# Kernel tuning notes

Hardware: AMD Instinct MI355X
Metric: run time of the kernel (lower is better)

## Reference

```python
import jax, jax.numpy as jnp
import numpy as np

# Hyperparameters from __init__ defaults / chosen init kwargs
GAMMA_NEG = 4.0
GAMMA_POS = 1.0
CLIP = 0.05
EPS = 1e-8
ALPHA1 = 2.0
ALPHA_OTHER = 0.5
TOP_K = 10

B, C = 2048, 9605


def setup_inputs() -> dict:
    key = jax.random.key(0)
    k_x, k_y, k_c, k_r, k_d, k_o = jax.random.split(key, 6)
    x = jax.random.normal(k_x, (B, C), dtype=jnp.float32)
    y = (jax.random.uniform(k_y, (B, C)) < 0.01).astype(jnp.float32)
    compost_idx = jax.random.randint(k_c, (30,), 0, C, dtype=jnp.int32)
    recycle_idx = jax.random.randint(k_r, (70,), 0, C, dtype=jnp.int32)
    donate_idx = jax.random.randint(k_d, (70,), 0, C, dtype=jnp.int32)
    other_idx = jax.random.randint(k_o, (40,), 0, C, dtype=jnp.int32)
    # dense whitelist mapping: 0 = not in W_human mapping; priority compost>recycle>donate
    wl_map = jnp.zeros((C,), dtype=jnp.int32)
    wl_map = wl_map.at[other_idx].set(4)
    wl_map = wl_map.at[donate_idx].set(3)
    wl_map = wl_map.at[recycle_idx].set(2)
    wl_map = wl_map.at[compost_idx].set(1)
    return {"x": x, "y": y, "compost_idx": compost_idx,
            "recycle_idx": recycle_idx, "donate_idx": donate_idx,
            "wl_map": wl_map}


def reference(x, y, compost_idx, recycle_idx, donate_idx, wl_map):
    b, c = x.shape
    xs_pos = jax.nn.sigmoid(x)
    xs_neg = jnp.minimum(1.0 - xs_pos + CLIP, 1.0)  # clip shift, clamp max=1
    # base asymmetric BCE term: y*log(p) + (1-y)*log(1-p+clip)
    base = (y * jnp.log(jnp.maximum(xs_pos, EPS))
            + (1.0 - y) * jnp.log(jnp.maximum(xs_neg, EPS)))  # [B, C]

    # per-sample ground-truth whitelist groups (find_gt_whitelist)
    has1 = jnp.sum(y[:, compost_idx], axis=1) > 0  # [B]
    has2 = jnp.sum(y[:, recycle_idx], axis=1) > 0
    has3 = jnp.sum(y[:, donate_idx], axis=1) > 0
    gt_only4 = ~(has1 | has2 | has3)  # gt_whitelist == [4]

    # top-10 predicted classes (argsort descending, first 10)
    _, top_idx = jax.lax.top_k(xs_pos, TOP_K)  # [B, 10]
    rows = jnp.arange(b)

    def step(carry, j):
        # j: [B] class index at current rank; sequential over rank (order matters)
        mult, found = carry
        wl = wl_map[j]                      # group id of this class, 0 if unmapped
        in_map = wl > 0
        in_gt = (((wl == 1) & has1) | ((wl == 2) & has2)
                 | ((wl == 3) & has3) | ((wl == 4) & gt_only4))
        f = jnp.where(in_map & gt_only4, ALPHA_OTHER, 1.0)
        f = f * jnp.where(in_map & (~in_gt) & (~found), ALPHA1, 1.0)
        mult = mult.at[rows, j].multiply(f)
        found = found | (in_map & in_gt)
        return (mult, found), None

    init = (jnp.ones((b, c), x.dtype), jnp.zeros((b,), dtype=bool))
    (mult, found), _ = jax.lax.scan(step, init, top_idx.T)  # scan over 10 ranks

    # if no gt-whitelist match found in top-10: multiply all top-10 by alpha1 again
    extra = jnp.where(found[:, None], 1.0, ALPHA1)  # [B, 1]
    mult = mult.at[rows[:, None], top_idx].multiply(
        jnp.broadcast_to(extra, (b, TOP_K)))

    # asymmetric focal weighting (computed without grad in original)
    pt = xs_pos * y + xs_neg * (1.0 - y)
    gamma = GAMMA_POS * y + GAMMA_NEG * (1.0 - y)
    w = jax.lax.stop_gradient(jnp.power(1.0 - pt, gamma))

    return -jnp.sum(base * mult * w)
```

## Files before the change

### kernel.cpp

```cpp
#include <hip/hip_runtime.h>

#define TOPK 10
#define CLIP 0.05f
#define EPSV 1e-8f
#define ALPHA1 2.0f
#define ALPHA_OTHER 0.5f
#define TCAND 2.5f
#define MAXC 512

__device__ __forceinline__ unsigned long long pack_vc(float v, int c, int C) {
  unsigned u = __float_as_uint(v);
  unsigned key = (u & 0x80000000u) ? ~u : (u | 0x80000000u);
  return ((unsigned long long)key << 32) | (unsigned)(C - c);
}
__device__ __forceinline__ float unpack_v(unsigned long long p) {
  unsigned key = (unsigned)(p >> 32);
  unsigned u = (key & 0x80000000u) ? (key & 0x7fffffffu) : ~key;
  return __uint_as_float(u);
}
__device__ __forceinline__ int unpack_c(unsigned long long p, int C) {
  return C - (int)(unsigned)(p & 0xffffffffu);
}

__device__ __forceinline__ float base_w(float xv, bool pos) {
  float p = 1.f / (1.f + __expf(-xv));
  float xneg = fminf(1.f - p + CLIP, 1.f);
  float q = pos ? p : xneg;
  float b = __logf(fmaxf(q, EPSV));
  float t = 1.f - q;
  float t2 = t * t;
  float w = pos ? t : t2 * t2;
  return b * w;
}

__global__ __launch_bounds__(256) void asl_kernel(
    const float* __restrict__ x, const float* __restrict__ y,
    const int* __restrict__ compost, const int* __restrict__ recycle,
    const int* __restrict__ donate, const int* __restrict__ wl_map,
    float* __restrict__ out, int C, int n1, int n2, int n3)
{
  const int row = blockIdx.x;
  const float* xr = x + (size_t)row * (size_t)C;
  const float* yr = y + (size_t)row * (size_t)C;
  const int tid = threadIdx.x;
  const int lane = tid & 63;
  const int wave = tid >> 6;

  __shared__ int s_has[3];
  __shared__ unsigned s_cnt;
  __shared__ unsigned long long s_cand[MAXC];
  __shared__ float s_sum[4];
  __shared__ unsigned long long s_top[TOPK];

  if (tid < 3) s_has[tid] = 0;
  if (tid == 0) s_cnt = 0;
  __syncthreads();

  const int ntot = n1 + n2 + n3;
  for (int i = tid; i < ntot; i += 256) {
    int which, colI;
    if (i < n1)            { which = 0; colI = compost[i]; }
    else if (i < n1 + n2)  { which = 1; colI = recycle[i - n1]; }
    else                   { which = 2; colI = donate[i - n1 - n2]; }
    if (yr[colI] > 0.5f) s_has[which] = 1;
  }

  float sum = 0.f;
#define PROCESS(XV, YV, COL)                                              \
  do {                                                                    \
    float _xv = (XV);                                                     \
    sum += base_w(_xv, (YV) > 0.5f);                                      \
    if (_xv > TCAND) {                                                    \
      unsigned _i = atomicAdd(&s_cnt, 1u);                                \
      if (_i < MAXC) s_cand[_i] = pack_vc(_xv, (COL), C);                 \
    }                                                                     \
  } while (0)

  int lead = (int)((4u - ((unsigned)((size_t)row * (size_t)C) & 3u)) & 3u);
  if (lead > C) lead = C;
  for (int col = tid; col < lead; col += 256) PROCESS(xr[col], yr[col], col);

  const int nvec = (C - lead) >> 2;
  const float4* __restrict__ x4 = (const float4*)(xr + lead);
  const float4* __restrict__ y4 = (const float4*)(yr + lead);
  for (int i = tid; i < nvec; i += 256) {
    float4 xv = x4[i];
    float4 yv = y4[i];
    int cb = lead + i * 4;
    PROCESS(xv.x, yv.x, cb + 0);
    PROCESS(xv.y, yv.y, cb + 1);
    PROCESS(xv.z, yv.z, cb + 2);
    PROCESS(xv.w, yv.w, cb + 3);
  }
  for (int col = lead + nvec * 4 + tid; col < C; col += 256)
    PROCESS(xr[col], yr[col], col);
#undef PROCESS

#pragma unroll
  for (int off = 32; off > 0; off >>= 1) sum += __shfl_xor(sum, off, 64);
  if (lane == 0) s_sum[wave] = sum;
  __syncthreads();

  if (wave == 0) {
    const unsigned cnt = s_cnt;
    unsigned long long ls[TOPK];
#pragma unroll
    for (int s = 0; s < TOPK; s++) ls[s] = 0ULL;

#define INSERT(P)                                                          \
    do {                                                                   \
      unsigned long long _p = (P);                                         \
      if (_p > ls[TOPK - 1]) {                                             \
        _Pragma("unroll")                                                  \
        for (int _s = 0; _s < TOPK; _s++) {                                \
          bool _g = _p > ls[_s];                                           \
          unsigned long long _t = _g ? ls[_s] : _p;                        \
          ls[_s] = _g ? _p : ls[_s];                                       \
          _p = _t;                                                         \
        }                                                                  \
      }                                                                    \
    } while (0)

    if (cnt >= TOPK && cnt <= MAXC) {
      for (unsigned i = lane; i < cnt; i += 64) INSERT(s_cand[i]);
    } else {
      for (int col = lane; col < C; col += 64) INSERT(pack_vc(xr[col], col, C));
    }
#undef INSERT

    for (int r = 0; r < TOPK; r++) {
      unsigned long long mine = ls[0];
      unsigned long long best = mine;
#pragma unroll
      for (int off = 32; off > 0; off >>= 1) {
        unsigned long long o = __shfl_xor(best, off, 64);
        best = (o > best) ? o : best;
      }
      if (lane == 0) s_top[r] = best;
      if (mine == best) {
#pragma unroll
        for (int s = 0; s < TOPK - 1; s++) ls[s] = ls[s + 1];
        ls[TOPK - 1] = 0ULL;
      }
    }
  }
  __syncthreads();

  if (tid == 0) {
    float total = s_sum[0] + s_sum[1] + s_sum[2] + s_sum[3];
    const bool h1 = s_has[0] != 0, h2 = s_has[1] != 0, h3 = s_has[2] != 0;
    const bool gt4 = !(h1 || h2 || h3);

    bool found = false;
    float fr[TOPK];
#pragma unroll
    for (int r = 0; r < TOPK; r++) {
      int col = unpack_c(s_top[r], C);
      int wl = wl_map[col];
      bool in_map = wl > 0;
      bool in_gt = (wl == 1 && h1) || (wl == 2 && h2) ||
                   (wl == 3 && h3) || (wl == 4 && gt4);
      float f = 1.f;
      if (in_map && gt4) f *= ALPHA_OTHER;
      if (in_map && !in_gt && !found) f *= ALPHA1;
      fr[r] = f;
      found = found || (in_map && in_gt);
    }
    const float extra = found ? 1.f : ALPHA1;
#pragma unroll
    for (int r = 0; r < TOPK; r++) {
      float mult = fr[r] * extra;
      if (mult != 1.f) {
        int col = unpack_c(s_top[r], C);
        float xv = unpack_v(s_top[r]);
        float bwv = base_w(xv, yr[col] > 0.5f);
        total += (mult - 1.f) * bwv;
      }
    }
    atomicAdd(out, -total);
  }
}

extern "C" void kernel_launch(void* const* d_in, const int* in_sizes, int n_in,
                              void* d_out, int out_size, void* d_ws, size_t ws_size,
                              hipStream_t stream) {
  const float* x       = (const float*)d_in[0];
  const float* y       = (const float*)d_in[1];
  const int*   compost = (const int*)d_in[2];
  const int*   recycle = (const int*)d_in[3];
  const int*   donate  = (const int*)d_in[4];
  const int*   wl_map  = (const int*)d_in[5];
  float* out = (float*)d_out;

  const int C  = in_sizes[5];
  const int B  = in_sizes[0] / C;
  const int n1 = in_sizes[2], n2 = in_sizes[3], n3 = in_sizes[4];

  hipMemsetAsync(out, 0, sizeof(float), stream);
  asl_kernel<<<B, 256, 0, stream>>>(x, y, compost, recycle, donate, wl_map,
                                    out, C, n1, n2, n3);
}
```

Before: 214.2 us.

## Batch four float4 loads per iteration and defer candidate pushes via bitmask

The main streaming loop now issues four independent float4 loads of x and y per iteration before computing, to raise memory-level parallelism. Candidate detection is reduced to a per-slot bitmask during the hot loop, and atomic pushes into the shared candidate list happen afterwards by re-reading the flagged vectors. The whitelist gather is also split so its first batch of loads is issued early and resolved later. The changes remove divergent atomics from the bandwidth-bound loop at the cost of more registers and a small re-read. The 32-bit mask caps each thread at 32 vector slots, which is enough for this row length but not for arbitrarily large C.

```diff
diff --git a/kernel.cpp b/kernel.cpp
--- a/kernel.cpp
+++ b/kernel.cpp
@@ -31,6 +31,16 @@
   float t2 = t * t;
   float w = pos ? t : t2 * t2;
   return b * w;
+}
+
+__device__ __forceinline__ void proc4(float4 X, float4 Y, float4& acc,
+                                      unsigned& cmask, int slot) {
+  acc.x += base_w(X.x, Y.x > 0.5f);
+  acc.y += base_w(X.y, Y.y > 0.5f);
+  acc.z += base_w(X.z, Y.z > 0.5f);
+  acc.w += base_w(X.w, Y.w > 0.5f);
+  float mx = fmaxf(fmaxf(X.x, X.y), fmaxf(X.z, X.w));
+  cmask |= (mx > TCAND ? 1u : 0u) << slot;
 }
 
 __global__ __launch_bounds__(256) void asl_kernel(
@@ -57,45 +67,84 @@
   __syncthreads();
 
   const int ntot = n1 + n2 + n3;
-  for (int i = tid; i < ntot; i += 256) {
-    int which, colI;
-    if (i < n1)            { which = 0; colI = compost[i]; }
-    else if (i < n1 + n2)  { which = 1; colI = recycle[i - n1]; }
-    else                   { which = 2; colI = donate[i - n1 - n2]; }
-    if (yr[colI] > 0.5f) s_has[which] = 1;
-  }
-
-  float sum = 0.f;
-#define PROCESS(XV, YV, COL)                                              \
+  float gflag = 0.f; int gwhich = -1;
+  if (tid < ntot) {
+    int colI;
+    if (tid < n1)           { gwhich = 0; colI = compost[tid]; }
+    else if (tid < n1 + n2) { gwhich = 1; colI = recycle[tid - n1]; }
+    else                    { gwhich = 2; colI = donate[tid - n1 - n2]; }
+    gflag = yr[colI];
+  }
+
+  float ssc = 0.f;
+
+#define PUSH(V, CCOL)                                                     \
+  do {                                                                    \
+    unsigned _i = atomicAdd(&s_cnt, 1u);                                  \
+    if (_i < MAXC) s_cand[_i] = pack_vc((V), (CCOL), C);                  \
+  } while (0)
+#define PROC_DIRECT(XV, YV, COL)                                          \
   do {                                                                    \
     float _xv = (XV);                                                     \
-    sum += base_w(_xv, (YV) > 0.5f);                                      \
-    if (_xv > TCAND) {                                                    \
-      unsigned _i = atomicAdd(&s_cnt, 1u);                                \
-      if (_i < MAXC) s_cand[_i] = pack_vc(_xv, (COL), C);                 \
-    }                                                                     \
+    ssc += base_w(_xv, (YV) > 0.5f);                                      \
+    if (_xv > TCAND) PUSH(_xv, (COL));                                    \
   } while (0)
 
   int lead = (int)((4u - ((unsigned)((size_t)row * (size_t)C) & 3u)) & 3u);
   if (lead > C) lead = C;
-  for (int col = tid; col < lead; col += 256) PROCESS(xr[col], yr[col], col);
+  for (int col = tid; col < lead; col += 256) PROC_DIRECT(xr[col], yr[col], col);
 
   const int nvec = (C - lead) >> 2;
   const float4* __restrict__ x4 = (const float4*)(xr + lead);
   const float4* __restrict__ y4 = (const float4*)(yr + lead);
-  for (int i = tid; i < nvec; i += 256) {
-    float4 xv = x4[i];
-    float4 yv = y4[i];
+
+  float4 sacc = make_float4(0.f, 0.f, 0.f, 0.f);
+  unsigned cmask = 0;
+
+  int slotbase = 0;
+  for (int base = tid; base < nvec; base += 1024, slotbase += 4) {
+    const bool v1 = base + 256 < nvec;
+    const bool v2 = base + 512 < nvec;
+    const bool v3 = base + 768 < nvec;
+    float4 xv0, xv1, xv2, xv3, yv0, yv1, yv2, yv3;
+    xv0 = x4[base];                 yv0 = y4[base];
+    if (v1) { xv1 = x4[base + 256]; yv1 = y4[base + 256]; }
+    if (v2) { xv2 = x4[base + 512]; yv2 = y4[base + 512]; }
+    if (v3) { xv3 = x4[base + 768]; yv3 = y4[base + 768]; }
+    proc4(xv0, yv0, sacc, cmask, slotbase + 0);
+    if (v1) proc4(xv1, yv1, sacc, cmask, slotbase + 1);
+    if (v2) proc4(xv2, yv2, sacc, cmask, slotbase + 2);
+    if (v3) proc4(xv3, yv3, sacc, cmask, slotbase + 3);
+  }
+
+  for (int col = lead + nvec * 4 + tid; col < C; col += 256)
+    PROC_DIRECT(xr[col], yr[col], col);
+
+  if (gwhich >= 0 && gflag > 0.5f) s_has[gwhich] = 1;
+  for (int i = 256 + tid; i < ntot; i += 256) {
+    int which, colI;
+    if (i < n1)           { which = 0; colI = compost[i]; }
+    else if (i < n1 + n2) { which = 1; colI = recycle[i - n1]; }
+    else                  { which = 2; colI = donate[i - n1 - n2]; }
+    if (yr[colI] > 0.5f) s_has[which] = 1;
+  }
+
+  while (cmask) {
+    int b = __ffs(cmask) - 1;
+    cmask &= cmask - 1;
+    int o = b >> 2, j = b & 3;
+    int i = tid + o * 1024 + j * 256;
+    float4 X = x4[i];
     int cb = lead + i * 4;
-    PROCESS(xv.x, yv.x, cb + 0);
-    PROCESS(xv.y, yv.y, cb + 1);
-    PROCESS(xv.z, yv.z, cb + 2);
-    PROCESS(xv.w, yv.w, cb + 3);
-  }
-  for (int col = lead + nvec * 4 + tid; col < C; col += 256)
-    PROCESS(xr[col], yr[col], col);
-#undef PROCESS
-
+    if (X.x > TCAND) PUSH(X.x, cb + 0);
+    if (X.y > TCAND) PUSH(X.y, cb + 1);
+    if (X.z > TCAND) PUSH(X.z, cb + 2);
+    if (X.w > TCAND) PUSH(X.w, cb + 3);
+  }
+#undef PROC_DIRECT
+#undef PUSH
+
+  float sum = ssc + sacc.x + sacc.y + sacc.z + sacc.w;
 #pragma unroll
   for (int off = 32; off > 0; off >>= 1) sum += __shfl_xor(sum, off, 64);
   if (lane == 0) s_sum[wave] = sum;
```

After: 205.8 us. 1.04x faster.

## Split into flat grid-stride streaming kernel plus per-row top-k fix kernel

Applied to the files above, without the earlier changes.

Replaces the one-block-per-row kernel with two kernels. The first streams x and y as one flat array over a fixed 1024-block grid, unrolled four ways, accumulating the loss and pushing top-k candidates into per-row global buffers with atomics. The second reads those candidates per row to find the top-10 and applies the multiplier correction. The aim is better memory-bandwidth use and load balance, at the cost of a second launch, an extra memset, global atomics and a double-precision division for each candidate's row index. It also switches the sigmoid to a hardware reciprocal and shrinks the candidate capacity to 128.

```diff
diff --git a/kernel.cpp b/kernel.cpp
--- a/kernel.cpp
+++ b/kernel.cpp
@@ -6,7 +6,7 @@
 #define ALPHA1 2.0f
 #define ALPHA_OTHER 0.5f
 #define TCAND 2.5f
-#define MAXC 512
+#define MAXC 128
 
 __device__ __forceinline__ unsigned long long pack_vc(float v, int c, int C) {
   unsigned u = __float_as_uint(v);
@@ -23,7 +23,8 @@
 }
 
 __device__ __forceinline__ float base_w(float xv, bool pos) {
-  float p = 1.f / (1.f + __expf(-xv));
+  float e = __expf(-xv);
+  float p = __builtin_amdgcn_rcpf(1.f + e);
   float xneg = fminf(1.f - p + CLIP, 1.f);
   float q = pos ? p : xneg;
   float b = __logf(fmaxf(q, EPSV));
@@ -33,11 +34,93 @@
   return b * w;
 }
 
-__global__ __launch_bounds__(256) void asl_kernel(
+__device__ __forceinline__ void push_cand(float v, long flat, int C, double invC,
+                                          int* __restrict__ cnt,
+                                          unsigned long long* __restrict__ cand,
+                                          int maxc) {
+  int row = (int)((double)flat * invC);
+  int col = (int)(flat - (long)row * (long)C);
+  if (col >= C) { row++; col -= C; }
+  if (col < 0)  { row--; col += C; }
+  int i = atomicAdd(&cnt[row], 1);
+  if (i < maxc) cand[(long)row * maxc + i] = pack_vc(v, col, C);
+}
+
+__device__ __forceinline__ void k1proc(float4 X, float4 Y, float4& acc, long flat,
+                                       int C, double invC, int* __restrict__ cnt,
+                                       unsigned long long* __restrict__ cand,
+                                       int maxc) {
+  acc.x += base_w(X.x, Y.x > 0.5f);
+  acc.y += base_w(X.y, Y.y > 0.5f);
+  acc.z += base_w(X.z, Y.z > 0.5f);
+  acc.w += base_w(X.w, Y.w > 0.5f);
+  float mx = fmaxf(fmaxf(X.x, X.y), fmaxf(X.z, X.w));
+  if (mx > TCAND) {
+    if (X.x > TCAND) push_cand(X.x, flat + 0, C, invC, cnt, cand, maxc);
+    if (X.y > TCAND) push_cand(X.y, flat + 1, C, invC, cnt, cand, maxc);
+    if (X.z > TCAND) push_cand(X.z, flat + 2, C, invC, cnt, cand, maxc);
+    if (X.w > TCAND) push_cand(X.w, flat + 3, C, invC, cnt, cand, maxc);
+  }
+}
+
+__global__ __launch_bounds__(256) void stream_kernel(
+    const float* __restrict__ x, const float* __restrict__ y,
+    float* __restrict__ out, int* __restrict__ cnt,
+    unsigned long long* __restrict__ cand, long N, int C, double invC, int maxc)
+{
+  const long N4 = N >> 2;
+  const long S = (long)gridDim.x * 256;
+  const long gtid = (long)blockIdx.x * 256 + threadIdx.x;
+  const float4* __restrict__ x4 = (const float4*)x;
+  const float4* __restrict__ y4 = (const float4*)y;
+
+  float4 a0 = make_float4(0.f, 0.f, 0.f, 0.f);
+  float4 a1 = make_float4(0.f, 0.f, 0.f, 0.f);
+  float4 a2 = make_float4(0.f, 0.f, 0.f, 0.f);
+  float4 a3 = make_float4(0.f, 0.f, 0.f, 0.f);
+
+  long i = gtid;
+  for (; i + 3 * S < N4; i += 4 * S) {
+    float4 X0 = x4[i];         float4 Y0 = y4[i];
+    float4 X1 = x4[i + S];     float4 Y1 = y4[i + S];
+    float4 X2 = x4[i + 2 * S]; float4 Y2 = y4[i + 2 * S];
+    float4 X3 = x4[i + 3 * S]; float4 Y3 = y4[i + 3 * S];
+    k1proc(X0, Y0, a0, 4 * i,           C, invC, cnt, cand, maxc);
+    k1proc(X1, Y1, a1, 4 * (i + S),     C, invC, cnt, cand, maxc);
+    k1proc(X2, Y2, a2, 4 * (i + 2 * S), C, invC, cnt, cand, maxc);
+    k1proc(X3, Y3, a3, 4 * (i + 3 * S), C, invC, cnt, cand, maxc);
+  }
+  for (; i < N4; i += S) {
+    float4 X = x4[i]; float4 Y = y4[i];
+    k1proc(X, Y, a0, 4 * i, C, invC, cnt, cand, maxc);
+  }
+  float sum = (a0.x + a0.y + a0.z + a0.w) + (a1.x + a1.y + a1.z + a1.w)
+            + (a2.x + a2.y + a2.z + a2.w) + (a3.x + a3.y + a3.z + a3.w);
+  if (gtid == 0) {
+    for (long j = N4 * 4; j < N; j++) {
+      float xv = x[j];
+      sum += base_w(xv, y[j] > 0.5f);
+      if (xv > TCAND) push_cand(xv, j, C, invC, cnt, cand, maxc);
+    }
+  }
+
+#pragma unroll
+  for (int off = 32; off > 0; off >>= 1) sum += __shfl_xor(sum, off, 64);
+  __shared__ float s_sum[4];
+  const int lane = threadIdx.x & 63, wave = threadIdx.x >> 6;
+  if (lane == 0) s_sum[wave] = sum;
+  __syncthreads();
+  if (threadIdx.x == 0)
+    atomicAdd(out, -(s_sum[0] + s_sum[1] + s_sum[2] + s_sum[3]));
+}
+
+__global__ __launch_bounds__(256) void fix_kernel(
     const float* __restrict__ x, const float* __restrict__ y,
     const int* __restrict__ compost, const int* __restrict__ recycle,
     const int* __restrict__ donate, const int* __restrict__ wl_map,
-    float* __restrict__ out, int C, int n1, int n2, int n3)
+    float* __restrict__ out, const int* __restrict__ cnt,
+    const unsigned long long* __restrict__ cand,
+    int C, int n1, int n2, int n3, int maxc)
 {
   const int row = blockIdx.x;
   const float* xr = x + (size_t)row * (size_t)C;
@@ -47,62 +130,24 @@
   const int wave = tid >> 6;
 
   __shared__ int s_has[3];
-  __shared__ unsigned s_cnt;
-  __shared__ unsigned long long s_cand[MAXC];
-  __shared__ float s_sum[4];
   __shared__ unsigned long long s_top[TOPK];
 
   if (tid < 3) s_has[tid] = 0;
-  if (tid == 0) s_cnt = 0;
   __syncthreads();
 
   const int ntot = n1 + n2 + n3;
-  for (int i = tid; i < ntot; i += 256) {
-    int which, colI;
-    if (i < n1)            { which = 0; colI = compost[i]; }
-    else if (i < n1 + n2)  { which = 1; colI = recycle[i - n1]; }
-    else                   { which = 2; colI = donate[i - n1 - n2]; }
-    if (yr[colI] > 0.5f) s_has[which] = 1;
-  }
-
-  float sum = 0.f;
-#define PROCESS(XV, YV, COL)                                              \
-  do {                                                                    \
-    float _xv = (XV);                                                     \
-    sum += base_w(_xv, (YV) > 0.5f);                                      \
-    if (_xv > TCAND) {                                                    \
-      unsigned _i = atomicAdd(&s_cnt, 1u);                                \
-      if (_i < MAXC) s_cand[_i] = pack_vc(_xv, (COL), C);                 \
-    }                                                                     \
-  } while (0)
-
-  int lead = (int)((4u - ((unsigned)((size_t)row * (size_t)C) & 3u)) & 3u);
-  if (lead > C) lead = C;
-  for (int col = tid; col < lead; col += 256) PROCESS(xr[col], yr[col], col);
-
-  const int nvec = (C - lead) >> 2;
-  const float4* __restrict__ x4 = (const float4*)(xr + lead);
-  const float4* __restrict__ y4 = (const float4*)(yr + lead);
-  for (int i = tid; i < nvec; i += 256) {
-    float4 xv = x4[i];
-    float4 yv = y4[i];
-    int cb = lead + i * 4;
-    PROCESS(xv.x, yv.x, cb + 0);
-    PROCESS(xv.y, yv.y, cb + 1);
-    PROCESS(xv.z, yv.z, cb + 2);
-    PROCESS(xv.w, yv.w, cb + 3);
-  }
-  for (int col = lead + nvec * 4 + tid; col < C; col += 256)
-    PROCESS(xr[col], yr[col], col);
-#undef PROCESS
-
-#pragma unroll
-  for (int off = 32; off > 0; off >>= 1) sum += __shfl_xor(sum, off, 64);
-  if (lane == 0) s_sum[wave] = sum;
-  __syncthreads();
+  if (wave > 0) {
+    for (int i = tid - 64; i < ntot; i += 192) {
+      int which, colI;
+      if (i < n1)           { which = 0; colI = compost[i]; }
+      else if (i < n1 + n2) { which = 1; colI = recycle[i - n1]; }
+      else                  { which = 2; colI = donate[i - n1 - n2]; }
+      if (yr[colI] > 0.5f) s_has[which] = 1;
+    }
+  }
 
   if (wave == 0) {
-    const unsigned cnt = s_cnt;
+    const int c = cnt[row];
     unsigned long long ls[TOPK];
 #pragma unroll
     for (int s = 0; s < TOPK; s++) ls[s] = 0ULL;
@@ -121,8 +166,9 @@
       }                                                                    \
     } while (0)
 
-    if (cnt >= TOPK && cnt <= MAXC) {
-      for (unsigned i = lane; i < cnt; i += 64) INSERT(s_cand[i]);
+    if (c >= TOPK && c <= maxc) {
+      const unsigned long long* cr = cand + (long)row * maxc;
+      for (int i = lane; i < c; i += 64) INSERT(cr[i]);
     } else {
       for (int col = lane; col < C; col += 64) INSERT(pack_vc(xr[col], col, C));
     }
@@ -147,7 +193,6 @@
   __syncthreads();
 
   if (tid == 0) {
-    float total = s_sum[0] + s_sum[1] + s_sum[2] + s_sum[3];
     const bool h1 = s_has[0] != 0, h2 = s_has[1] != 0, h3 = s_has[2] != 0;
     const bool gt4 = !(h1 || h2 || h3);
 
@@ -167,17 +212,17 @@
       found = found || (in_map && in_gt);
     }
     const float extra = found ? 1.f : ALPHA1;
+    float total = 0.f;
 #pragma unroll
     for (int r = 0; r < TOPK; r++) {
       float mult = fr[r] * extra;
       if (mult != 1.f) {
         int col = unpack_c(s_top[r], C);
         float xv = unpack_v(s_top[r]);
-        float bwv = base_w(xv, yr[col] > 0.5f);
-        total += (mult - 1.f) * bwv;
+        total += (mult - 1.f) * base_w(xv, yr[col] > 0.5f);
       }
     }
-    atomicAdd(out, -total);
+    if (total != 0.f) atomicAdd(out, -total);
   }
 }
 
@@ -194,9 +239,22 @@
 
   const int C  = in_sizes[5];
   const int B  = in_sizes[0] / C;
+  const long N = (long)in_sizes[0];
   const int n1 = in_sizes[2], n2 = in_sizes[3], n3 = in_sizes[4];
 
+  size_t cand_off = ((size_t)B * 4 + 7) & ~(size_t)7;
+  int maxc = MAXC;
+  if (ws_size < cand_off + (size_t)B * maxc * 8) {
+    size_t fit = (ws_size > cand_off) ? (ws_size - cand_off) / ((size_t)B * 8) : 0;
+    maxc = (int)fit;
+  }
+  int* cnt = (int*)d_ws;
+  unsigned long long* cand = (unsigned long long*)((char*)d_ws + cand_off);
+  double invC = 1.0 / (double)C;
+
   hipMemsetAsync(out, 0, sizeof(float), stream);
-  asl_kernel<<<B, 256, 0, stream>>>(x, y, compost, recycle, donate, wl_map,
-                                    out, C, n1, n2, n3);
-}
+  hipMemsetAsync(cnt, 0, (size_t)B * 4, stream);
+  stream_kernel<<<1024, 256, 0, stream>>>(x, y, out, cnt, cand, N, C, invC, maxc);
+  fix_kernel<<<B, 256, 0, stream>>>(x, y, compost, recycle, donate, wl_map,
+                                    out, cnt, cand, C, n1, n2, n3, maxc);
+}
```

Result: slower. 246.6 us (+15.1%).
